# Kernel tuning notes

Hardware: AMD Instinct MI355X
Metric: run time of the kernel (lower is better)

The kernel has to match this reference:

```python
import jax, jax.numpy as jnp
import numpy as np

D_MODEL = 1024
NUM_HEADS = 16
HEAD_DIM = D_MODEL // NUM_HEADS


def setup_inputs() -> dict:
    key = jax.random.key(0)
    k1, k2, k3, k4, k5 = jax.random.split(key, 5)
    B, S = 2, 2048
    X = jax.random.normal(k1, (B, S, D_MODEL), dtype=jnp.float32)
    Wqkv = jax.random.normal(k2, (3 * D_MODEL, D_MODEL), dtype=jnp.float32) * 0.02
    bqkv = jax.random.normal(k3, (3 * D_MODEL,), dtype=jnp.float32) * 0.02
    Wo = jax.random.normal(k4, (D_MODEL, D_MODEL), dtype=jnp.float32) * 0.02
    bo = jax.random.normal(k5, (D_MODEL,), dtype=jnp.float32) * 0.02
    return {"X": X, "Wqkv": Wqkv, "bqkv": bqkv, "Wo": Wo, "bo": bo}


def reference(X, Wqkv, bqkv, Wo, bo):
    B, S, D = X.shape
    # fused QKV projection (torch Linear: x @ W.T + b)
    qkv = X @ Wqkv.T + bqkv                                  # [B, S, 3D]
    qkv = qkv.reshape(B, S, NUM_HEADS, 3 * HEAD_DIM)
    qkv = jnp.transpose(qkv, (0, 2, 1, 3))                   # [B, H, S, 3*hd]
    q, k, v = jnp.split(qkv, 3, axis=-1)                     # each [B, H, S, hd]
    # naive scaled dot-product attention (materializes full SxS scores)
    scale = 1.0 / jnp.sqrt(jnp.asarray(HEAD_DIM, dtype=X.dtype))
    scores = jnp.einsum("bhqd,bhkd->bhqk", q, k) * scale     # [B, H, S, S]
    attn = jax.nn.softmax(scores, axis=-1)
    values = jnp.einsum("bhqk,bhkd->bhqd", attn, v)          # [B, H, S, hd]
    values = jnp.transpose(values, (0, 2, 1, 3)).reshape(B, S, D)
    return values @ Wo.T + bo
```

## Files before the change

kernel.cpp:

```cpp
#include <hip/hip_runtime.h>

#define DM    1024
#define NH    16
#define HD    64
#define SEQ   2048
#define BATCH 2
#define NQKV  3072
#define MTOT  4096

using half2v = __attribute__((ext_vector_type(2))) _Float16;
using half4  = __attribute__((ext_vector_type(4))) _Float16;
using half8  = __attribute__((ext_vector_type(8))) _Float16;
using f32x4  = __attribute__((ext_vector_type(4))) float;

typedef const __attribute__((address_space(1))) unsigned int* gp_t;
typedef __attribute__((address_space(3))) unsigned int* lp_t;

__device__ __forceinline__ void gl2lds16(const void* g, void* l) {
    __builtin_amdgcn_global_load_lds((gp_t)g, (lp_t)l, 16, 0, 0);
}

__device__ __forceinline__ f32x4 fzero4() {
    f32x4 v; v[0] = 0.f; v[1] = 0.f; v[2] = 0.f; v[3] = 0.f; return v;
}

__device__ __forceinline__ int sw8(int row, int col) {
    return (row << 6) | ((((col >> 3) ^ row) & 7) << 3) | (col & 7);
}

#define CSCALE 0.18033688011112042f

__device__ __forceinline__ half2v expp2(float a, float b) {
    return __builtin_bit_cast(half2v, __builtin_amdgcn_cvt_pkrtz(
        __builtin_amdgcn_exp2f(a), __builtin_amdgcn_exp2f(b)));
}

__global__ __launch_bounds__(256) void cvt_all(const float* __restrict__ X,
                                               const float* __restrict__ W1,
                                               const float* __restrict__ W2,
                                               const float* __restrict__ bqkv,
                                               float* __restrict__ bscaled,
                                               _Float16* __restrict__ out) {
    const int nX = MTOT * DM / 4, nW1 = NQKV * DM / 4, nW2 = DM * DM / 4;
    int i = blockIdx.x * 256 + threadIdx.x;
    if (i < NQKV) {
        const float b = bqkv[i];
        bscaled[i] = ((i % 192) < 64) ? b * CSCALE : b;
    }
    if (i >= nX + nW1 + nW2) return;
    float4 f;
    float sc = 1.0f;
    if (i < nX) {
        f = reinterpret_cast<const float4*>(X)[i];
    } else if (i < nX + nW1) {
        const int off = i - nX;
        f = reinterpret_cast<const float4*>(W1)[off];
        const int row = off >> 8;
        if ((row % 192) < 64) sc = CSCALE;
    } else {
        f = reinterpret_cast<const float4*>(W2)[i - nX - nW1];
    }
    half4 h;
    h[0] = (_Float16)(f.x * sc); h[1] = (_Float16)(f.y * sc);
    h[2] = (_Float16)(f.z * sc); h[3] = (_Float16)(f.w * sc);
    reinterpret_cast<half4*>(out)[i] = h;
}

template <bool OUT_F16>
__global__ __launch_bounds__(256) void gemm_nt(const _Float16* __restrict__ A,
                                               const _Float16* __restrict__ B,
                                               const float* __restrict__ bias,
                                               void* __restrict__ Cout,
                                               int M, int N, int K) {
    __shared__ _Float16 lA[128 * 64];
    __shared__ _Float16 lB[128 * 64];
    const int tid = threadIdx.x;
    const int m0 = blockIdx.y * 128, n0 = blockIdx.x * 128;
    const int wave = tid >> 6, lane = tid & 63, quad = lane >> 4, l15 = lane & 15;
    const int wm = (wave & 1) * 64, wn = (wave >> 1) * 64;

    f32x4 acc[4][4];
#pragma unroll
    for (int i = 0; i < 4; ++i)
#pragma unroll
        for (int j = 0; j < 4; ++j) acc[i][j] = fzero4();

    const int cperm = (((tid & 7) ^ (tid >> 3)) & 7) * 8;
    const _Float16* Ab = A + (long)(m0 + (tid >> 3)) * K + cperm;
    const _Float16* Bb = B + (long)(n0 + (tid >> 3)) * K + cperm;
    char* lAp = (char*)lA + tid * 16;
    char* lBp = (char*)lB + tid * 16;

    for (int kt = 0; kt < K; kt += 64) {
        __syncthreads();
#pragma unroll
        for (int j = 0; j < 4; ++j) {
            gl2lds16(Ab + (long)j * 32 * K + kt, lAp + j * 4096);
            gl2lds16(Bb + (long)j * 32 * K + kt, lBp + j * 4096);
        }
        __syncthreads();
#pragma unroll
        for (int ks = 0; ks < 2; ++ks) {
            half8 af[4], bfr[4];
#pragma unroll
            for (int t = 0; t < 4; ++t) {
                af[t]  = *(const half8*)(lA + sw8(wm + t * 16 + l15, ks * 32 + quad * 8));
                bfr[t] = *(const half8*)(lB + sw8(wn + t * 16 + l15, ks * 32 + quad * 8));
            }
#pragma unroll
            for (int mt = 0; mt < 4; ++mt)
#pragma unroll
                for (int nt = 0; nt < 4; ++nt)
                    acc[mt][nt] = __builtin_amdgcn_mfma_f32_16x16x32_f16(
                        af[mt], bfr[nt], acc[mt][nt], 0, 0, 0);
        }
    }

    float bs[4];
#pragma unroll
    for (int nt = 0; nt < 4; ++nt) bs[nt] = bias[n0 + wn + nt * 16 + l15];

#pragma unroll
    for (int mt = 0; mt < 4; ++mt) {
#pragma unroll
        for (int r = 0; r < 4; ++r) {
            const int m = m0 + wm + mt * 16 + quad * 4 + r;
#pragma unroll
            for (int nt = 0; nt < 4; ++nt) {
                const int n = n0 + wn + nt * 16 + l15;
                const float v = acc[mt][nt][r] + bs[nt];
                if constexpr (OUT_F16)
                    ((_Float16*)Cout)[(long)m * N + n] = (_Float16)v;
                else
                    ((float*)Cout)[(long)m * N + n] = v;
            }
        }
    }
}

template <bool OUT_F16>
__global__ __launch_bounds__(256) void gemm_nt_64(const _Float16* __restrict__ A,
                                                  const _Float16* __restrict__ B,
                                                  const float* __restrict__ bias,
                                                  void* __restrict__ Cout,
                                                  int M, int N, int K) {
    __shared__ _Float16 lA[64 * 64];
    __shared__ _Float16 lB[128 * 64];
    const int tid = threadIdx.x;
    const int m0 = blockIdx.y * 64, n0 = blockIdx.x * 128;
    const int wave = tid >> 6, lane = tid & 63, quad = lane >> 4, l15 = lane & 15;
    const int wm = (wave & 1) * 32, wn = (wave >> 1) * 64;

    f32x4 acc[2][4];
#pragma unroll
    for (int i = 0; i < 2; ++i)
#pragma unroll
        for (int j = 0; j < 4; ++j) acc[i][j] = fzero4();

    const int cperm = (((tid & 7) ^ (tid >> 3)) & 7) * 8;
    const _Float16* Ab = A + (long)(m0 + (tid >> 3)) * K + cperm;
    const _Float16* Bb = B + (long)(n0 + (tid >> 3)) * K + cperm;
    char* lAp = (char*)lA + tid * 16;
    char* lBp = (char*)lB + tid * 16;

    for (int kt = 0; kt < K; kt += 64) {
        __syncthreads();
#pragma unroll
        for (int j = 0; j < 2; ++j)
            gl2lds16(Ab + (long)j * 32 * K + kt, lAp + j * 4096);
#pragma unroll
        for (int j = 0; j < 4; ++j)
            gl2lds16(Bb + (long)j * 32 * K + kt, lBp + j * 4096);
        __syncthreads();
#pragma unroll
        for (int ks = 0; ks < 2; ++ks) {
            half8 af[2], bfr[4];
#pragma unroll
            for (int t = 0; t < 2; ++t)
                af[t] = *(const half8*)(lA + sw8(wm + t * 16 + l15, ks * 32 + quad * 8));
#pragma unroll
            for (int t = 0; t < 4; ++t)
                bfr[t] = *(const half8*)(lB + sw8(wn + t * 16 + l15, ks * 32 + quad * 8));
#pragma unroll
            for (int mt = 0; mt < 2; ++mt)
#pragma unroll
                for (int nt = 0; nt < 4; ++nt)
                    acc[mt][nt] = __builtin_amdgcn_mfma_f32_16x16x32_f16(
                        af[mt], bfr[nt], acc[mt][nt], 0, 0, 0);
        }
    }

    float bs[4];
#pragma unroll
    for (int nt = 0; nt < 4; ++nt) bs[nt] = bias[n0 + wn + nt * 16 + l15];

#pragma unroll
    for (int mt = 0; mt < 2; ++mt) {
#pragma unroll
        for (int r = 0; r < 4; ++r) {
            const int m = m0 + wm + mt * 16 + quad * 4 + r;
#pragma unroll
            for (int nt = 0; nt < 4; ++nt) {
                const int n = n0 + wn + nt * 16 + l15;
                const float v = acc[mt][nt][r] + bs[nt];
                if constexpr (OUT_F16)
                    ((_Float16*)Cout)[(long)m * N + n] = (_Float16)v;
                else
                    ((float*)Cout)[(long)m * N + n] = v;
            }
        }
    }
}

__global__ __launch_bounds__(256) void repack_v(const _Float16* __restrict__ qkvh,
                                                _Float16* __restrict__ vt) {
    const int b = blockIdx.z, h = blockIdx.y, s0 = blockIdx.x * 32;
    const int d = threadIdx.x & 63, si = threadIdx.x >> 6;
    const _Float16* src = qkvh + (long)(b * SEQ + s0) * NQKV + h * 192 + 128 + d;
    half8 v;
#pragma unroll
    for (int hi = 0; hi < 2; ++hi)
#pragma unroll
        for (int r = 0; r < 4; ++r)
            v[hi * 4 + r] = src[(long)(hi * 16 + si * 4 + r) * NQKV];
    *(half8*)(vt + (long)((b * NH + h) * HD + d) * SEQ + s0 + si * 8) = v;
}

__global__ __launch_bounds__(256) void attn_flash(const _Float16* __restrict__ qkv,
                                                  const _Float16* __restrict__ vt,
                                                  _Float16* __restrict__ aout) {
    __shared__ _Float16 lKV[4][64 * 64];

    const int L = blockIdx.x + 16 * blockIdx.y + 256 * blockIdx.z;
    const int c = L & 7, j = L >> 3;
    const int pair = c * 4 + (j >> 4);
    const int b = pair >> 4, h = pair & 15;
    const int q0 = (j & 15) * 128;

    const int tid = threadIdx.x;
    const int wave = tid >> 6, lane = tid & 63, quad = lane >> 4, l15 = lane & 15;
    const int cperm8 = (((tid & 7) ^ (tid >> 3)) & 7) * 8;

    const _Float16* qsrc = qkv + (long)(b * SEQ + q0 + (tid >> 3)) * NQKV + h * 192 + cperm8;
#pragma unroll
    for (int jq = 0; jq < 4; ++jq)
        gl2lds16(qsrc + (long)jq * 32 * NQKV, (char*)lKV + jq * 4096 + tid * 16);
    __syncthreads();

    half8 qf[2][2];
#pragma unroll
    for (int qt = 0; qt < 2; ++qt)
#pragma unroll
        for (int ks = 0; ks < 2; ++ks)
            qf[qt][ks] = *(const half8*)(lKV[0] + sw8(wave * 32 + qt * 16 + l15, ks * 32 + quad * 8));
    __syncthreads();

    f32x4 O[2][4];
#pragma unroll
    for (int qt = 0; qt < 2; ++qt)
#pragma unroll
        for (int dt = 0; dt < 4; ++dt) O[qt][dt] = fzero4();
    f32x4 lsum[2] = {fzero4(), fzero4()};

    half8 ones;
#pragma unroll
    for (int i = 0; i < 8; ++i) ones[i] = (_Float16)1.0f;

    const _Float16* ksrc = qkv + (long)(b * SEQ + (tid >> 3)) * NQKV + h * 192 + 64 + cperm8;
    const _Float16* vsrc = vt + (long)((b * NH + h) * HD + (tid >> 3)) * SEQ + cperm8;

#pragma unroll
    for (int jj = 0; jj < 2; ++jj) {
        gl2lds16(ksrc + (long)(jj * 32) * NQKV, (char*)lKV[0] + jj * 4096 + tid * 16);
        gl2lds16(vsrc + (long)(jj * 32) * SEQ,  (char*)lKV[2] + jj * 4096 + tid * 16);
    }
    __syncthreads();

    for (int it = 0; it < 32; ++it) {
        const int cur = it & 1;
        if (it < 31) {
            const int s0n = (it + 1) * 64;
#pragma unroll
            for (int jj = 0; jj < 2; ++jj) {
                gl2lds16(ksrc + (long)(s0n + jj * 32) * NQKV, (char*)lKV[cur ^ 1] + jj * 4096 + tid * 16);
                gl2lds16(vsrc + (long)(jj * 32) * SEQ + s0n,  (char*)lKV[2 + (cur ^ 1)] + jj * 4096 + tid * 16);
            }
        }
        const _Float16* lK = lKV[cur];
        const _Float16* lV = lKV[2 + cur];

#pragma unroll
        for (int t = 0; t < 2; ++t) {
            f32x4 s[2][2];
            s[0][0] = fzero4(); s[0][1] = fzero4();
            s[1][0] = fzero4(); s[1][1] = fzero4();
#pragma unroll
            for (int tt = 0; tt < 2; ++tt) {
#pragma unroll
                for (int ks = 0; ks < 2; ++ks) {
                    half8 kf = *(const half8*)(lK + sw8((2 * t + tt) * 16 + l15, ks * 32 + quad * 8));
                    s[0][tt] = __builtin_amdgcn_mfma_f32_16x16x32_f16(kf, qf[0][ks], s[0][tt], 0, 0, 0);
                    s[1][tt] = __builtin_amdgcn_mfma_f32_16x16x32_f16(kf, qf[1][ks], s[1][tt], 0, 0, 0);
                }
            }
            half8 pf[2];
#pragma unroll
            for (int qt = 0; qt < 2; ++qt) {
                half2v p01 = expp2(s[qt][0][0], s[qt][0][1]);
                half2v p23 = expp2(s[qt][0][2], s[qt][0][3]);
                half2v p45 = expp2(s[qt][1][0], s[qt][1][1]);
                half2v p67 = expp2(s[qt][1][2], s[qt][1][3]);
                half4 lo = __builtin_shufflevector(p01, p23, 0, 1, 2, 3);
                half4 hi = __builtin_shufflevector(p45, p67, 0, 1, 2, 3);
                pf[qt] = __builtin_shufflevector(lo, hi, 0, 1, 2, 3, 4, 5, 6, 7);
                lsum[qt] = __builtin_amdgcn_mfma_f32_16x16x32_f16(pf[qt], ones, lsum[qt], 0, 0, 0);
            }
#pragma unroll
            for (int dt = 0; dt < 4; ++dt) {
                half8 vf = *(const half8*)(lV + sw8(dt * 16 + l15, t * 32 + quad * 8));
                O[0][dt] = __builtin_amdgcn_mfma_f32_16x16x32_f16(pf[0], vf, O[0][dt], 0, 0, 0);
                O[1][dt] = __builtin_amdgcn_mfma_f32_16x16x32_f16(pf[1], vf, O[1][dt], 0, 0, 0);
            }
        }
        __syncthreads();
    }

#pragma unroll
    for (int qt = 0; qt < 2; ++qt) {
#pragma unroll
        for (int r = 0; r < 4; ++r) {
            const float lr = 1.0f / lsum[qt][r];
            const int row = b * SEQ + q0 + wave * 32 + qt * 16 + quad * 4 + r;
#pragma unroll
            for (int dt = 0; dt < 4; ++dt)
                aout[(long)row * DM + h * HD + dt * 16 + l15] =
                    (_Float16)(O[qt][dt][r] * lr);
        }
    }
}

extern "C" void kernel_launch(void* const* d_in, const int* in_sizes, int n_in,
                              void* d_out, int out_size, void* d_ws, size_t ws_size,
                              hipStream_t stream) {
    const float* X    = (const float*)d_in[0];
    const float* Wqkv = (const float*)d_in[1];
    const float* bqkv = (const float*)d_in[2];
    const float* Wo   = (const float*)d_in[3];
    const float* bo   = (const float*)d_in[4];

    char* ws = (char*)d_ws;
    _Float16* Xh   = (_Float16*)(ws);
    _Float16* Wqh  = (_Float16*)(ws + (size_t)8  * 1048576);
    _Float16* Woh  = (_Float16*)(ws + (size_t)14 * 1048576);
    _Float16* qkvh = (_Float16*)(ws + (size_t)16 * 1048576);
    _Float16* vth  = (_Float16*)(ws + (size_t)40 * 1048576);
    _Float16* atth = (_Float16*)(ws + (size_t)48 * 1048576);
    float* bscaled = (float*)(ws + (size_t)48 * 1048576);

    const int ncvt = (MTOT * DM + NQKV * DM + DM * DM) / 4;
    cvt_all<<<(ncvt + 255) / 256, 256, 0, stream>>>(X, Wqkv, Wo, bqkv, bscaled, Xh);

    gemm_nt<true><<<dim3(NQKV / 128, MTOT / 128), 256, 0, stream>>>(
        Xh, Wqh, bscaled, qkvh, MTOT, NQKV, DM);

    repack_v<<<dim3(SEQ / 32, NH, BATCH), 256, 0, stream>>>(qkvh, vth);

    attn_flash<<<dim3(SEQ / 128, NH, BATCH), 256, 0, stream>>>(qkvh, vth, atth);

    gemm_nt_64<false><<<dim3(DM / 128, MTOT / 64), 256, 0, stream>>>(
        atth, Woh, bo, d_out, MTOT, DM, DM);
}
```

Measured before the change: 185.0 us.

## Triple-buffer K/V tiles in flash attention with partial vmcnt waits

The attention loop moves from double to triple buffering of the K and V tiles in LDS, prefetching two tiles ahead. Each iteration waits only for the oldest outstanding global-to-LDS loads (vmcnt(8)) rather than all of them, with explicit barriers and sched_barriers replacing __syncthreads. The goal is to hide global load latency behind MFMA work. It raises LDS use from 32KB to 48KB per block, which could lower occupancy, and it depends on exact vmcnt counting for correctness.

```diff
diff --git a/kernel.cpp b/kernel.cpp
--- a/kernel.cpp
+++ b/kernel.cpp
@@ -34,6 +34,19 @@
     return __builtin_bit_cast(half2v, __builtin_amdgcn_cvt_pkrtz(
         __builtin_amdgcn_exp2f(a), __builtin_amdgcn_exp2f(b)));
 }
+
+#define ACQ(N) do {                                             \
+    asm volatile("s_waitcnt vmcnt(" #N ")" ::: "memory");       \
+    __builtin_amdgcn_sched_barrier(0);                          \
+    __builtin_amdgcn_s_barrier();                               \
+    __builtin_amdgcn_sched_barrier(0);                          \
+} while (0)
+#define REL() do {                                              \
+    __builtin_amdgcn_sched_barrier(0);                          \
+    asm volatile("s_waitcnt lgkmcnt(0)" ::: "memory");          \
+    __builtin_amdgcn_s_barrier();                               \
+    __builtin_amdgcn_sched_barrier(0);                          \
+} while (0)
 
 __global__ __launch_bounds__(256) void cvt_all(const float* __restrict__ X,
                                                const float* __restrict__ W1,
@@ -229,7 +242,7 @@
 __global__ __launch_bounds__(256) void attn_flash(const _Float16* __restrict__ qkv,
                                                   const _Float16* __restrict__ vt,
                                                   _Float16* __restrict__ aout) {
-    __shared__ _Float16 lKV[4][64 * 64];
+    __shared__ _Float16 lbuf[6][64 * 64];
 
     const int L = blockIdx.x + 16 * blockIdx.y + 256 * blockIdx.z;
     const int c = L & 7, j = L >> 3;
@@ -240,11 +253,12 @@
     const int tid = threadIdx.x;
     const int wave = tid >> 6, lane = tid & 63, quad = lane >> 4, l15 = lane & 15;
     const int cperm8 = (((tid & 7) ^ (tid >> 3)) & 7) * 8;
-
-    const _Float16* qsrc = qkv + (long)(b * SEQ + q0 + (tid >> 3)) * NQKV + h * 192 + cperm8;
+    const int srow = tid >> 3;
+
+    const _Float16* qsrc = qkv + (long)(b * SEQ + q0 + srow) * NQKV + h * 192 + cperm8;
 #pragma unroll
     for (int jq = 0; jq < 4; ++jq)
-        gl2lds16(qsrc + (long)jq * 32 * NQKV, (char*)lKV + jq * 4096 + tid * 16);
+        gl2lds16(qsrc + (long)jq * 32 * NQKV, (char*)lbuf + jq * 4096 + tid * 16);
     __syncthreads();
 
     half8 qf[2][2];
@@ -252,7 +266,8 @@
     for (int qt = 0; qt < 2; ++qt)
 #pragma unroll
         for (int ks = 0; ks < 2; ++ks)
-            qf[qt][ks] = *(const half8*)(lKV[0] + sw8(wave * 32 + qt * 16 + l15, ks * 32 + quad * 8));
+            qf[qt][ks] = *(const half8*)((const _Float16*)lbuf +
+                             sw8(wave * 32 + qt * 16 + l15, ks * 32 + quad * 8));
     __syncthreads();
 
     f32x4 O[2][4];
@@ -266,43 +281,34 @@
 #pragma unroll
     for (int i = 0; i < 8; ++i) ones[i] = (_Float16)1.0f;
 
-    const _Float16* ksrc = qkv + (long)(b * SEQ + (tid >> 3)) * NQKV + h * 192 + 64 + cperm8;
-    const _Float16* vsrc = vt + (long)((b * NH + h) * HD + (tid >> 3)) * SEQ + cperm8;
+    const _Float16* ksrc = qkv + (long)(b * SEQ + srow) * NQKV + h * 192 + 64 + cperm8;
+    const _Float16* vsrc = vt + (long)((b * NH + h) * HD + srow) * SEQ + cperm8;
 
 #pragma unroll
     for (int jj = 0; jj < 2; ++jj) {
-        gl2lds16(ksrc + (long)(jj * 32) * NQKV, (char*)lKV[0] + jj * 4096 + tid * 16);
-        gl2lds16(vsrc + (long)(jj * 32) * SEQ,  (char*)lKV[2] + jj * 4096 + tid * 16);
-    }
-    __syncthreads();
-
-    for (int it = 0; it < 32; ++it) {
-        const int cur = it & 1;
-        if (it < 31) {
-            const int s0n = (it + 1) * 64;
-#pragma unroll
-            for (int jj = 0; jj < 2; ++jj) {
-                gl2lds16(ksrc + (long)(s0n + jj * 32) * NQKV, (char*)lKV[cur ^ 1] + jj * 4096 + tid * 16);
-                gl2lds16(vsrc + (long)(jj * 32) * SEQ + s0n,  (char*)lKV[2 + (cur ^ 1)] + jj * 4096 + tid * 16);
-            }
-        }
-        const _Float16* lK = lKV[cur];
-        const _Float16* lV = lKV[2 + cur];
-
+        gl2lds16(ksrc + (long)(jj * 32) * NQKV, (char*)lbuf[0] + jj * 4096 + tid * 16);
+        gl2lds16(vsrc + (long)(jj * 32) * SEQ,  (char*)lbuf[3] + jj * 4096 + tid * 16);
+    }
+#pragma unroll
+    for (int jj = 0; jj < 2; ++jj) {
+        gl2lds16(ksrc + (long)(64 + jj * 32) * NQKV, (char*)lbuf[1] + jj * 4096 + tid * 16);
+        gl2lds16(vsrc + (long)(jj * 32) * SEQ + 64,  (char*)lbuf[4] + jj * 4096 + tid * 16);
+    }
+
+    auto compute = [&](const _Float16* lK, const _Float16* lV) {
 #pragma unroll
         for (int t = 0; t < 2; ++t) {
             f32x4 s[2][2];
             s[0][0] = fzero4(); s[0][1] = fzero4();
             s[1][0] = fzero4(); s[1][1] = fzero4();
 #pragma unroll
-            for (int tt = 0; tt < 2; ++tt) {
+            for (int tt = 0; tt < 2; ++tt)
 #pragma unroll
                 for (int ks = 0; ks < 2; ++ks) {
                     half8 kf = *(const half8*)(lK + sw8((2 * t + tt) * 16 + l15, ks * 32 + quad * 8));
                     s[0][tt] = __builtin_amdgcn_mfma_f32_16x16x32_f16(kf, qf[0][ks], s[0][tt], 0, 0, 0);
                     s[1][tt] = __builtin_amdgcn_mfma_f32_16x16x32_f16(kf, qf[1][ks], s[1][tt], 0, 0, 0);
                 }
-            }
             half8 pf[2];
 #pragma unroll
             for (int qt = 0; qt < 2; ++qt) {
@@ -322,8 +328,28 @@
                 O[1][dt] = __builtin_amdgcn_mfma_f32_16x16x32_f16(pf[1], vf, O[1][dt], 0, 0, 0);
             }
         }
-        __syncthreads();
-    }
+    };
+
+    int cur = 0;
+    for (int it = 0; it < 30; ++it) {
+        int pre = cur + 2; if (pre >= 3) pre -= 3;
+        const long s0n = (long)(it + 2) * 64;
+#pragma unroll
+        for (int jj = 0; jj < 2; ++jj) {
+            gl2lds16(ksrc + (s0n + jj * 32) * NQKV,     (char*)lbuf[pre] + jj * 4096 + tid * 16);
+            gl2lds16(vsrc + (long)(jj * 32) * SEQ + s0n, (char*)lbuf[3 + pre] + jj * 4096 + tid * 16);
+        }
+        ACQ(8);
+        compute(lbuf[cur], lbuf[3 + cur]);
+        REL();
+        cur = (cur == 2) ? 0 : cur + 1;
+    }
+    ACQ(4);
+    compute(lbuf[cur], lbuf[3 + cur]);
+    REL();
+    cur = (cur == 2) ? 0 : cur + 1;
+    ACQ(0);
+    compute(lbuf[cur], lbuf[3 + cur]);
 
 #pragma unroll
     for (int qt = 0; qt < 2; ++qt) {
```

New measurement: 196.1 us. 1.06x slower.
